# Kernel tuning notes

Hardware: AMD Instinct MI355X
Metric: run time of the kernel (lower is better)

The kernel has to match this reference:

```python
import jax, jax.numpy as jnp
import numpy as np

N_NODES = 50000
BN_EPS = 1e-5


def gcn_conv(x, W, b, src, dst):
    # PyG GCNConv: linear, add self-loops, symmetric degree normalization, scatter-add, bias.
    h = x @ W                                        # [N, D]
    n = x.shape[0]
    deg = jax.ops.segment_sum(jnp.ones(src.shape[0], x.dtype), dst,
                              num_segments=n) + 1.0  # +1 for self-loop
    dinv = jnp.where(deg > 0, jax.lax.rsqrt(deg), 0.0)
    norm = dinv[src] * dinv[dst]                     # [E]
    agg = jax.ops.segment_sum(h[src] * norm[:, None], dst, num_segments=n)
    agg = agg + h * (dinv * dinv)[:, None]           # self-loop contribution
    return agg + b


def batch_norm(x, gamma, beta):
    # training-mode BN over the node axis (biased variance, as torch)
    mu = jnp.mean(x, axis=0)
    var = jnp.mean((x - mu) ** 2, axis=0)
    return (x - mu) * jax.lax.rsqrt(var + BN_EPS) * gamma + beta


def setup_inputs() -> dict:
    key = jax.random.key(0)
    ks = jax.random.split(key, 8)
    D, C = 128, 10
    x = jax.random.normal(ks[0], (N_NODES, D), dtype=jnp.float32)
    edge_index = jax.random.randint(ks[1], (2, 640000), 0, N_NODES, dtype=jnp.int32)
    s = 1.0 / np.sqrt(D)
    return {
        "x": x,
        "edge_index": edge_index,
        "W1": jax.random.normal(ks[2], (D, D), dtype=jnp.float32) * s,
        "b1": jnp.zeros((D,), jnp.float32),
        "gamma1": jnp.ones((D,), jnp.float32),
        "beta1": jnp.zeros((D,), jnp.float32),
        "W2": jax.random.normal(ks[3], (D, D), dtype=jnp.float32) * s,
        "b2": jnp.zeros((D,), jnp.float32),
        "gamma2": jnp.ones((D,), jnp.float32),
        "beta2": jnp.zeros((D,), jnp.float32),
        "lin1_w": jax.random.normal(ks[4], (D, D), dtype=jnp.float32) * s,
        "lin1_b": jnp.zeros((D,), jnp.float32),
        "lin2_w": jax.random.normal(ks[5], (D, C), dtype=jnp.float32) * s,
        "lin2_b": jnp.zeros((C,), jnp.float32),
    }


def reference(x, edge_index, W1, b1, gamma1, beta1, W2, b2, gamma2, beta2,
              lin1_w, lin1_b, lin2_w, lin2_b):
    src, dst = edge_index[0], edge_index[1]
    # layer 1: GCNConv -> ReLU -> BN (dropout = identity at eval)
    h = jax.nn.relu(gcn_conv(x, W1, b1, src, dst))
    h = batch_norm(h, gamma1, beta1)
    # layer 2
    h = jax.nn.relu(gcn_conv(h, W2, b2, src, dst))
    h = batch_norm(h, gamma2, beta2)
    # MLP head
    h = jax.nn.relu(h @ lin1_w + lin1_b)
    logits = h @ lin2_w + lin2_b
    return jax.nn.log_softmax(logits, axis=-1)
```

## Files before the change

### kernel.cpp

```cpp
#include <hip/hip_runtime.h>
#include <hip/hip_bf16.h>
#include <math.h>

typedef unsigned int uint;
typedef unsigned short ushort;
using f32x4 = __attribute__((ext_vector_type(4))) float;
using s16x8 = __attribute__((ext_vector_type(8))) short;

#define NSLOT 64

__device__ __forceinline__ float bflo(uint u) { return __uint_as_float(u << 16); }
__device__ __forceinline__ float bfhi(uint u) { return __uint_as_float(u & 0xffff0000u); }
__device__ __forceinline__ ushort f2bf(float f) {
    uint u = __float_as_uint(f);
    return (ushort)((u + 0x7fffu + ((u >> 16) & 1u)) >> 16);
}
__device__ __forceinline__ float sel4f(float a, float b, float c, float d, int i) {
    float r = a; r = (i == 1) ? b : r; r = (i == 2) ? c : r; r = (i == 3) ? d : r; return r;
}
__device__ __forceinline__ int sel4i(int a, int b, int c, int d, int i) {
    int r = a; r = (i == 1) ? b : r; r = (i == 2) ? c : r; r = (i == 3) ? d : r; return r;
}


__global__ void deg_count(const int* __restrict__ dst, int* __restrict__ deg, int E) {
    int e0 = blockIdx.x * 512 + threadIdx.x;
    int e1 = e0 + 256;
    if (e1 < E) {
        int dA = dst[e0], dB = dst[e1];
        atomicAdd(&deg[dA], 1);
        atomicAdd(&deg[dB], 1);
    } else if (e0 < E) {
        atomicAdd(&deg[dst[e0]], 1);
    }
}

__global__ __launch_bounds__(256) void deg_block_sum(const int* __restrict__ deg,
                                                     int* __restrict__ bsum, int N) {
    __shared__ int s[256];
    int i = blockIdx.x * 256 + threadIdx.x;
    s[threadIdx.x] = (i < N) ? deg[i] : 0;
    __syncthreads();
    #pragma unroll
    for (int off = 128; off > 0; off >>= 1) {
        if (threadIdx.x < off) s[threadIdx.x] += s[threadIdx.x + off];
        __syncthreads();
    }
    if (threadIdx.x == 0) bsum[blockIdx.x] = s[0];
}

__global__ __launch_bounds__(256) void fill_rowstart(const int* __restrict__ deg,
                                                     const int* __restrict__ bsum,
                                                     int* __restrict__ row_start,
                                                     int* __restrict__ cursor,
                                                     float* __restrict__ dinv,
                                                     int N, int E, int nblk) {
    __shared__ int s[256];
    __shared__ int sb[256];
    int t = threadIdx.x;
    int i = blockIdx.x * 256 + t;
    int dg = (i < N) ? deg[i] : 0;
    s[t] = dg;
    sb[t] = (t < nblk) ? bsum[t] : 0;
    __syncthreads();
    for (int off = 1; off < 256; off <<= 1) {
        int v1 = (t >= off) ? s[t - off] : 0;
        int v2 = (t >= off) ? sb[t - off] : 0;
        __syncthreads();
        s[t] += v1;
        sb[t] += v2;
        __syncthreads();
    }
    if (i < N) {
        int boff = (blockIdx.x == 0) ? 0 : sb[blockIdx.x - 1];
        int excl = boff + s[t] - dg;
        row_start[i] = excl;
        cursor[i] = excl;
        dinv[i] = rsqrtf((float)dg + 1.0f);
    }
    if (i == 0) row_start[N] = E;
}

__global__ void csr_fill(const int* __restrict__ src, const int* __restrict__ dst,
                         int* __restrict__ cursor, int* __restrict__ csr_src, int E) {
    int e0 = blockIdx.x * 512 + threadIdx.x;
    int e1 = e0 + 256;
    if (e1 < E) {
        int sA = src[e0], dA = dst[e0];
        int sB = src[e1], dB = dst[e1];
        int pA = atomicAdd(&cursor[dA], 1);
        int pB = atomicAdd(&cursor[dB], 1);
        csr_src[pA] = sA;
        csr_src[pB] = sB;
    } else if (e0 < E) {
        int s = src[e0], d = dst[e0];
        int p = atomicAdd(&cursor[d], 1);
        csr_src[p] = s;
    }
}


__global__ __launch_bounds__(256) void prep_weights(const float* __restrict__ W1,
                                                    const float* __restrict__ W2,
                                                    const float* __restrict__ W3,
                                                    const float* __restrict__ l2w,
                                                    const float* __restrict__ l2b,
                                                    ushort* __restrict__ wt1,
                                                    ushort* __restrict__ wt2,
                                                    ushort* __restrict__ wt3,
                                                    ushort* __restrict__ w2bf,
                                                    float* __restrict__ b2pad) {
    int i = blockIdx.x * 256 + threadIdx.x;
    int li = i & 16383;
    int k = li >> 7, n = li & 127;
    const float* Ws = (i < 16384) ? W1 : (i < 32768) ? W2 : W3;
    ushort* Wd = (i < 16384) ? wt1 : (i < 32768) ? wt2 : wt3;
    Wd[n * 128 + k] = f2bf(Ws[li]);
    if (i < 2048) {
        int c = i >> 7, kk = i & 127;
        float v = (c < 10) ? l2w[kk * 10 + c] : 0.f;
        w2bf[c * 128 + kk] = f2bf(v);
    }
    if (i < 16) b2pad[i] = (i < 10) ? l2b[i] : -1e30f;
}


template<bool XF32, bool AFF, bool PRESCALE, bool HEAD>
__global__ __launch_bounds__(256) void gemm_mfma(const void* __restrict__ Xv,
                                                 const float* __restrict__ scale,
                                                 const float* __restrict__ shift,
                                                 const ushort* __restrict__ Bt,
                                                 const float* __restrict__ bias,
                                                 const float* __restrict__ dinv,
                                                 ushort* __restrict__ Y,
                                                 const ushort* __restrict__ W2bf,
                                                 const float* __restrict__ b2pad,
                                                 float* __restrict__ OUT, int N) {
    __shared__ char smem[2 * 16384 + 32768];
    char* Bl = smem + 32768;

    int tid = threadIdx.x;
    int brow = blockIdx.x * 128;

    {
        int n = tid >> 1, h = tid & 1;
        const uint4* srcp = (const uint4*)(Bt + n * 128 + h * 64);
        #pragma unroll
        for (int i = 0; i < 8; ++i) {
            uint4 v = srcp[i];
            int u = (h * 8 + i) ^ (n & 7);
            *(uint4*)(Bl + n * 256 + u * 16) = v;
        }
    }

    int lane = tid & 63, w = tid >> 6;
    int m = lane & 15, g = lane >> 4;
    int wr = w * 16;

    #pragma unroll
    for (int t = 0; t < 2; ++t) {
        char* Al = smem + t * 16384;
        int rbase = brow + t * 64;

        {
            int r = tid >> 2, c0 = (tid & 3) * 32;
            int row = rbase + r;
            bool ok = row < N;
            uint pk[16];
            if (XF32) {
                const float* Xr = (const float*)Xv + (size_t)row * 128 + c0;
                #pragma unroll
                for (int i = 0; i < 16; ++i) {
                    float f0 = ok ? Xr[i * 2] : 0.f;
                    float f1 = ok ? Xr[i * 2 + 1] : 0.f;
                    pk[i] = (uint)f2bf(f0) | ((uint)f2bf(f1) << 16);
                }
            } else {
                const uint* Xr = (const uint*)((const ushort*)Xv + (size_t)row * 128 + c0);
                #pragma unroll
                for (int i = 0; i < 16; ++i) {
                    uint u = ok ? Xr[i] : 0u;
                    float f0 = bflo(u), f1 = bfhi(u);
                    if (AFF) {
                        int c = c0 + i * 2;
                        f0 = f0 * scale[c] + shift[c];
                        f1 = f1 * scale[c + 1] + shift[c + 1];
                    }
                    pk[i] = (uint)f2bf(f0) | ((uint)f2bf(f1) << 16);
                }
            }
            #pragma unroll
            for (int i = 0; i < 4; ++i) {
                int u = ((tid & 3) * 4 + i) ^ (r & 7);
                *(uint4*)(Al + r * 256 + u * 16) = *(uint4*)&pk[i * 4];
            }
        }
        __syncthreads();

        f32x4 acc[8];
        #pragma unroll
        for (int nt = 0; nt < 8; ++nt) acc[nt] = (f32x4){0.f, 0.f, 0.f, 0.f};

        #pragma unroll
        for (int kk = 0; kk < 4; ++kk) {
            int u = (kk * 4 + g) ^ (m & 7);
            s16x8 a = *(const s16x8*)(Al + (wr + m) * 256 + u * 16);
            #pragma unroll
            for (int nt = 0; nt < 8; ++nt) {
                s16x8 b = *(const s16x8*)(Bl + (nt * 16 + m) * 256 + u * 16);
                acc[nt] = __builtin_amdgcn_mfma_f32_16x16x32_bf16(a, b, acc[nt], 0, 0, 0);
            }
        }

        if (!HEAD) {
            #pragma unroll
            for (int i = 0; i < 4; ++i) {
                int row = rbase + wr + g * 4 + i;
                if (row < N) {
                    float dv = PRESCALE ? dinv[row] : 1.f;
                    #pragma unroll
                    for (int nt = 0; nt < 8; ++nt) {
                        float v = acc[nt][i];
                        if (PRESCALE) v *= dv;
                        Y[(size_t)row * 128 + nt * 16 + m] = f2bf(v);
                    }
                }
            }
        } else {
            float bv[8];
            #pragma unroll
            for (int nt = 0; nt < 8; ++nt) bv[nt] = bias[nt * 16 + m];
            #pragma unroll
            for (int i = 0; i < 4; ++i) {
                int r = wr + g * 4 + i;
                #pragma unroll
                for (int nt = 0; nt < 8; ++nt) {
                    float v = fmaxf(acc[nt][i] + bv[nt], 0.f);
                    int col = nt * 16 + m;
                    int u = (col >> 3) ^ (r & 7);
                    *(ushort*)(Al + r * 256 + u * 16 + (col & 7) * 2) = f2bf(v);
                }
            }
            __syncthreads();
            float b2v = b2pad[m];
            f32x4 lg = (f32x4){b2v, b2v, b2v, b2v};
            #pragma unroll
            for (int kk = 0; kk < 4; ++kk) {
                int u = (kk * 4 + g) ^ (m & 7);
                s16x8 a = *(const s16x8*)(Al + (wr + m) * 256 + u * 16);
                s16x8 b = *(const s16x8*)(&W2bf[m * 128 + (kk * 4 + g) * 8]);
                lg = __builtin_amdgcn_mfma_f32_16x16x32_bf16(a, b, lg, 0, 0, 0);
            }
            #pragma unroll
            for (int i = 0; i < 4; ++i) {
                float v = lg[i];
                float mx = v;
                #pragma unroll
                for (int off = 8; off > 0; off >>= 1) mx = fmaxf(mx, __shfl_xor(mx, off, 64));
                float ex = expf(v - mx);
                float sm = ex;
                #pragma unroll
                for (int off = 8; off > 0; off >>= 1) sm += __shfl_xor(sm, off, 64);
                float res = v - (mx + logf(sm));
                int grow = rbase + wr + g * 4 + i;
                if (m < 10 && grow < N) OUT[(size_t)grow * 10 + m] = res;
            }
        }
    }
}


__global__ __launch_bounds__(256) void gather_fused(const ushort* __restrict__ H,
                                                    const int* __restrict__ row_start,
                                                    const int* __restrict__ csr_src,
                                                    const float* __restrict__ dinv,
                                                    const float* __restrict__ bias,
                                                    ushort* __restrict__ Y,
                                                    float* __restrict__ bnpart, int N) {
    int g = threadIdx.x >> 6, lane = threadIdx.x & 63;
    int d = lane * 2;
    float b0 = bias[d], b1 = bias[d + 1];
    float s0 = 0.f, s1 = 0.f, ss0 = 0.f, ss1 = 0.f;

    int nchunks = (N + 3) / 4;
    int chunk = blockIdx.x * 4 + g;

    if (chunk < nchunks) {
        int c = chunk * 4;
        int nn = min(4, N - c);

        int rsv = row_start[c + min(lane, nn)];
        int rs0 = __shfl(rsv, 0);
        int rs1 = __shfl(rsv, min(1, nn));
        int rs2 = __shfl(rsv, min(2, nn));
        int rs3 = __shfl(rsv, min(3, nn));
        int rs4 = __shfl(rsv, nn);

        float dvv = dinv[c + min(lane, nn - 1)];
        float dv0 = __shfl(dvv, 0);
        float dv1 = __shfl(dvv, min(1, nn - 1));
        float dv2 = __shfl(dvv, min(2, nn - 1));
        float dv3 = __shfl(dvv, min(3, nn - 1));

        uint h0 = *(const uint*)&H[(size_t)c * 128 + d];
        uint h1 = (nn > 1) ? *(const uint*)&H[(size_t)(c + 1) * 128 + d] : 0u;
        uint h2 = (nn > 2) ? *(const uint*)&H[(size_t)(c + 2) * 128 + d] : 0u;
        uint h3 = (nn > 3) ? *(const uint*)&H[(size_t)(c + 3) * 128 + d] : 0u;

        float i0_0 = bflo(h0) * dv0 + b0, i1_0 = bfhi(h0) * dv0 + b1;
        float i0_1 = bflo(h1) * dv1 + b0, i1_1 = bfhi(h1) * dv1 + b1;
        float i0_2 = bflo(h2) * dv2 + b0, i1_2 = bfhi(h2) * dv2 + b1;
        float i0_3 = bflo(h3) * dv3 + b0, i1_3 = bfhi(h3) * dv3 + b1;

        int e0 = rs0, eend = rs4;
        int seg = 0;
        int nextb = rs1;
        float i0s = i0_0, i1s = i1_0, dvs = dv0;
        float es0 = 0.f, es1 = 0.f;

        for (int base = e0; base < eend; base += 64) {
            int cnt = min(64, eend - base);
            int sl = (lane < cnt) ? csr_src[base + lane] : 0;

            for (int j = 0; j < cnt; j += 16) {
                int mm = min(16, cnt - j);
                uint v[16];
                #pragma unroll
                for (int k = 0; k < 16; ++k) {
                    int idx = min(j + k, cnt - 1);
                    int sk = __shfl(sl, idx);
                    v[k] = *(const uint*)&H[(size_t)sk * 128 + d];
                }
                #pragma unroll
                for (int k = 0; k < 16; ++k) {
                    if (k < mm) {
                        int e = base + j + k;
                        while (e >= nextb) {
                            float r0 = fmaxf(es0 * dvs + i0s, 0.f);
                            float r1 = fmaxf(es1 * dvs + i1s, 0.f);
                            *(uint*)&Y[(size_t)(c + seg) * 128 + d] =
                                (uint)f2bf(r0) | ((uint)f2bf(r1) << 16);
                            s0 += r0; ss0 += r0 * r0; s1 += r1; ss1 += r1 * r1;
                            seg++;
                            i0s = sel4f(i0_0, i0_1, i0_2, i0_3, seg);
                            i1s = sel4f(i1_0, i1_1, i1_2, i1_3, seg);
                            dvs = sel4f(dv0, dv1, dv2, dv3, seg);
                            nextb = sel4i(rs1, rs2, rs3, rs4, seg);
                            es0 = 0.f; es1 = 0.f;
                        }
                        es0 += bflo(v[k]);
                        es1 += bfhi(v[k]);
                    }
                }
            }
        }
        for (;;) {
            float r0 = fmaxf(es0 * dvs + i0s, 0.f);
            float r1 = fmaxf(es1 * dvs + i1s, 0.f);
            *(uint*)&Y[(size_t)(c + seg) * 128 + d] = (uint)f2bf(r0) | ((uint)f2bf(r1) << 16);
            s0 += r0; ss0 += r0 * r0; s1 += r1; ss1 += r1 * r1;
            seg++;
            if (seg >= nn) break;
            i0s = sel4f(i0_0, i0_1, i0_2, i0_3, seg);
            i1s = sel4f(i1_0, i1_1, i1_2, i1_3, seg);
            dvs = sel4f(dv0, dv1, dv2, dv3, seg);
            nextb = sel4i(rs1, rs2, rs3, rs4, seg);
            es0 = 0.f; es1 = 0.f;
        }
    }

    float* bp = bnpart + (size_t)(blockIdx.x & (NSLOT - 1)) * 256;
    __shared__ float red[4][128];
    red[g][d] = s0; red[g][d + 1] = s1;
    __syncthreads();
    if (g == 0) {
        atomicAdd(&bp[d],     red[0][d] + red[1][d] + red[2][d] + red[3][d]);
        atomicAdd(&bp[d + 1], red[0][d + 1] + red[1][d + 1] + red[2][d + 1] + red[3][d + 1]);
    }
    __syncthreads();
    red[g][d] = ss0; red[g][d + 1] = ss1;
    __syncthreads();
    if (g == 0) {
        atomicAdd(&bp[128 + d],     red[0][d] + red[1][d] + red[2][d] + red[3][d]);
        atomicAdd(&bp[128 + d + 1], red[0][d + 1] + red[1][d + 1] + red[2][d + 1] + red[3][d + 1]);
    }
}

__global__ void bnfinalize(float* __restrict__ bnpart,
                           const float* __restrict__ gamma, const float* __restrict__ beta,
                           float* __restrict__ scale, float* __restrict__ shift, float invN) {
    int d = threadIdx.x;
    float sum = 0.f, ss = 0.f;
    #pragma unroll 8
    for (int s = 0; s < NSLOT; ++s) {
        sum += bnpart[s * 256 + d];
        ss  += bnpart[s * 256 + 128 + d];
        bnpart[s * 256 + d] = 0.f;
        bnpart[s * 256 + 128 + d] = 0.f;
    }
    float mu  = sum * invN;
    float var = ss * invN - mu * mu;
    float sc  = gamma[d] * rsqrtf(var + 1e-5f);
    scale[d] = sc;
    shift[d] = beta[d] - mu * sc;
}


static inline char* align16(char* p) { return (char*)(((uintptr_t)p + 15) & ~(uintptr_t)15); }

extern "C" void kernel_launch(void* const* d_in, const int* in_sizes, int n_in,
                              void* d_out, int out_size, void* d_ws, size_t ws_size,
                              hipStream_t stream) {
    const float* x    = (const float*)d_in[0];
    const int*   ei   = (const int*)d_in[1];
    const float* W1   = (const float*)d_in[2];
    const float* b1   = (const float*)d_in[3];
    const float* g1   = (const float*)d_in[4];
    const float* be1  = (const float*)d_in[5];
    const float* W2   = (const float*)d_in[6];
    const float* b2   = (const float*)d_in[7];
    const float* g2   = (const float*)d_in[8];
    const float* be2  = (const float*)d_in[9];
    const float* l1w  = (const float*)d_in[10];
    const float* l1b  = (const float*)d_in[11];
    const float* l2w  = (const float*)d_in[12];
    const float* l2b  = (const float*)d_in[13];
    float* out = (float*)d_out;

    int N = in_sizes[0] / 128;
    int E = in_sizes[1] / 2;
    const int* srcp = ei;
    const int* dstp = ei + E;

    char* w = (char*)d_ws;
    ushort* bufA   = (ushort*)w;  w = align16(w + (size_t)N * 128 * 2);
    ushort* bufB   = (ushort*)w;  w = align16(w + (size_t)N * 128 * 2);
    int*   degc    = (int*)w;     w += (size_t)N * 4;
    float* bnpart  = (float*)w;   w = align16(w + (size_t)NSLOT * 256 * 4);
    float* dinv    = (float*)w;   w = align16(w + (size_t)N * 4);
    int*   row_st  = (int*)w;     w = align16(w + (size_t)(N + 1) * 4);
    int*   cursor  = (int*)w;     w = align16(w + (size_t)N * 4);
    int*   bsum    = (int*)w;     w = align16(w + 256 * 4);
    int*   csr_src = (int*)w;     w = align16(w + (size_t)E * 4);
    float* scale   = (float*)w;   w = align16(w + 128 * 4);
    float* shift   = (float*)w;   w = align16(w + 128 * 4);
    ushort* wt1    = (ushort*)w;  w = align16(w + 16384 * 2);
    ushort* wt2    = (ushort*)w;  w = align16(w + 16384 * 2);
    ushort* wt3    = (ushort*)w;  w = align16(w + 16384 * 2);
    ushort* w2bf   = (ushort*)w;  w = align16(w + 2048 * 2);
    float* b2pad   = (float*)w;   w = align16(w + 16 * 4);

    int eg2 = (E + 511) / 512;
    int ng = (N + 255) / 256;
    int gemm_grid = (N + 127) / 128;
    int nchunks = (N + 3) / 4;
    int gather_grid = (nchunks + 3) / 4;

    hipMemsetAsync(degc, 0, ((size_t)N + NSLOT * 256) * 4, stream);
    deg_count<<<eg2, 256, 0, stream>>>(dstp, degc, E);
    deg_block_sum<<<ng, 256, 0, stream>>>(degc, bsum, N);
    fill_rowstart<<<ng, 256, 0, stream>>>(degc, bsum, row_st, cursor, dinv, N, E, ng);
    csr_fill<<<eg2, 256, 0, stream>>>(srcp, dstp, cursor, csr_src, E);
    prep_weights<<<192, 256, 0, stream>>>(W1, W2, l1w, l2w, l2b, wt1, wt2, wt3, w2bf, b2pad);

    gemm_mfma<true, false, true, false><<<gemm_grid, 256, 0, stream>>>(
        x, nullptr, nullptr, wt1, nullptr, dinv, bufA, nullptr, nullptr, nullptr, N);
    gather_fused<<<gather_grid, 256, 0, stream>>>(bufA, row_st, csr_src, dinv, b1, bufB, bnpart, N);
    bnfinalize<<<1, 128, 0, stream>>>(bnpart, g1, be1, scale, shift, 1.0f / N);

    gemm_mfma<false, true, true, false><<<gemm_grid, 256, 0, stream>>>(
        bufB, scale, shift, wt2, nullptr, dinv, bufA, nullptr, nullptr, nullptr, N);
    gather_fused<<<gather_grid, 256, 0, stream>>>(bufA, row_st, csr_src, dinv, b2, bufB, bnpart, N);
    bnfinalize<<<1, 128, 0, stream>>>(bnpart, g2, be2, scale, shift, 1.0f / N);

    gemm_mfma<false, true, false, true><<<gemm_grid, 256, 0, stream>>>(
        bufB, scale, shift, wt3, l1b, nullptr, nullptr, w2bf, b2pad, out, N);
}
```

Before: 323.3 us.

## Cut kernel launches by fusing memset, scan, and BN finalize into neighbouring kernels

Replaces the memset and weight-prep launches with a single init kernel that zeroes the counters and converts the weights. The two scan kernels become one, using a global spin barrier across blocks. BN finalize moves into the gather kernel through a last-block-done counter. Edge kernels now handle four edges per thread. This removes several small launches, but the spin barrier only works if all scan blocks are resident at once, and the last-block reduction adds serial work at the end of the gather.

```diff
diff --git a/kernel.cpp b/kernel.cpp
--- a/kernel.cpp
+++ b/kernel.cpp
@@ -23,94 +23,24 @@
 }
 
 
-__global__ void deg_count(const int* __restrict__ dst, int* __restrict__ deg, int E) {
-    int e0 = blockIdx.x * 512 + threadIdx.x;
-    int e1 = e0 + 256;
-    if (e1 < E) {
-        int dA = dst[e0], dB = dst[e1];
-        atomicAdd(&deg[dA], 1);
-        atomicAdd(&deg[dB], 1);
-    } else if (e0 < E) {
-        atomicAdd(&deg[dst[e0]], 1);
-    }
-}
-
-__global__ __launch_bounds__(256) void deg_block_sum(const int* __restrict__ deg,
-                                                     int* __restrict__ bsum, int N) {
-    __shared__ int s[256];
-    int i = blockIdx.x * 256 + threadIdx.x;
-    s[threadIdx.x] = (i < N) ? deg[i] : 0;
-    __syncthreads();
-    #pragma unroll
-    for (int off = 128; off > 0; off >>= 1) {
-        if (threadIdx.x < off) s[threadIdx.x] += s[threadIdx.x + off];
-        __syncthreads();
-    }
-    if (threadIdx.x == 0) bsum[blockIdx.x] = s[0];
-}
-
-__global__ __launch_bounds__(256) void fill_rowstart(const int* __restrict__ deg,
-                                                     const int* __restrict__ bsum,
-                                                     int* __restrict__ row_start,
-                                                     int* __restrict__ cursor,
-                                                     float* __restrict__ dinv,
-                                                     int N, int E, int nblk) {
-    __shared__ int s[256];
-    __shared__ int sb[256];
-    int t = threadIdx.x;
-    int i = blockIdx.x * 256 + t;
-    int dg = (i < N) ? deg[i] : 0;
-    s[t] = dg;
-    sb[t] = (t < nblk) ? bsum[t] : 0;
-    __syncthreads();
-    for (int off = 1; off < 256; off <<= 1) {
-        int v1 = (t >= off) ? s[t - off] : 0;
-        int v2 = (t >= off) ? sb[t - off] : 0;
-        __syncthreads();
-        s[t] += v1;
-        sb[t] += v2;
-        __syncthreads();
-    }
-    if (i < N) {
-        int boff = (blockIdx.x == 0) ? 0 : sb[blockIdx.x - 1];
-        int excl = boff + s[t] - dg;
-        row_start[i] = excl;
-        cursor[i] = excl;
-        dinv[i] = rsqrtf((float)dg + 1.0f);
-    }
-    if (i == 0) row_start[N] = E;
-}
-
-__global__ void csr_fill(const int* __restrict__ src, const int* __restrict__ dst,
-                         int* __restrict__ cursor, int* __restrict__ csr_src, int E) {
-    int e0 = blockIdx.x * 512 + threadIdx.x;
-    int e1 = e0 + 256;
-    if (e1 < E) {
-        int sA = src[e0], dA = dst[e0];
-        int sB = src[e1], dB = dst[e1];
-        int pA = atomicAdd(&cursor[dA], 1);
-        int pB = atomicAdd(&cursor[dB], 1);
-        csr_src[pA] = sA;
-        csr_src[pB] = sB;
-    } else if (e0 < E) {
-        int s = src[e0], d = dst[e0];
-        int p = atomicAdd(&cursor[d], 1);
-        csr_src[p] = s;
-    }
-}
-
-
-__global__ __launch_bounds__(256) void prep_weights(const float* __restrict__ W1,
-                                                    const float* __restrict__ W2,
-                                                    const float* __restrict__ W3,
-                                                    const float* __restrict__ l2w,
-                                                    const float* __restrict__ l2b,
-                                                    ushort* __restrict__ wt1,
-                                                    ushort* __restrict__ wt2,
-                                                    ushort* __restrict__ wt3,
-                                                    ushort* __restrict__ w2bf,
-                                                    float* __restrict__ b2pad) {
-    int i = blockIdx.x * 256 + threadIdx.x;
+__global__ __launch_bounds__(256) void init_prep(uint4* __restrict__ zbase, int nz, int ZB,
+                                                 const float* __restrict__ W1,
+                                                 const float* __restrict__ W2,
+                                                 const float* __restrict__ W3,
+                                                 const float* __restrict__ l2w,
+                                                 const float* __restrict__ l2b,
+                                                 ushort* __restrict__ wt1,
+                                                 ushort* __restrict__ wt2,
+                                                 ushort* __restrict__ wt3,
+                                                 ushort* __restrict__ w2bf,
+                                                 float* __restrict__ b2pad) {
+    int bid = blockIdx.x;
+    if (bid < ZB) {
+        int i = bid * 256 + threadIdx.x;
+        if (i < nz) zbase[i] = (uint4){0u, 0u, 0u, 0u};
+        return;
+    }
+    int i = (bid - ZB) * 256 + threadIdx.x;
     int li = i & 16383;
     int k = li >> 7, n = li & 127;
     const float* Ws = (i < 16384) ? W1 : (i < 32768) ? W2 : W3;
@@ -122,6 +52,92 @@
         w2bf[c * 128 + kk] = f2bf(v);
     }
     if (i < 16) b2pad[i] = (i < 10) ? l2b[i] : -1e30f;
+}
+
+
+__global__ __launch_bounds__(256) void deg_count(const int* __restrict__ dst,
+                                                 int* __restrict__ deg, int E) {
+    int base = blockIdx.x * 1024 + threadIdx.x;
+    int d[4]; bool ok[4];
+    #pragma unroll
+    for (int k = 0; k < 4; ++k) {
+        int e = base + k * 256;
+        ok[k] = e < E;
+        d[k] = ok[k] ? dst[e] : 0;
+    }
+    #pragma unroll
+    for (int k = 0; k < 4; ++k)
+        if (ok[k]) atomicAdd(&deg[d[k]], 1);
+}
+
+
+__global__ __launch_bounds__(256) void scan_fill(const int* __restrict__ deg,
+                                                 int* __restrict__ bsum,
+                                                 int* __restrict__ sync_ctr,
+                                                 int* __restrict__ row_start,
+                                                 int* __restrict__ cursor,
+                                                 float* __restrict__ dinv,
+                                                 int N, int E, int nblk) {
+    __shared__ int s[256];
+    __shared__ int sb[256];
+    int t = threadIdx.x;
+    int bid = blockIdx.x;
+    int i = bid * 256 + t;
+    int dg = (i < N) ? deg[i] : 0;
+    s[t] = dg;
+    __syncthreads();
+    for (int off = 1; off < 256; off <<= 1) {
+        int v = (t >= off) ? s[t - off] : 0;
+        __syncthreads();
+        s[t] += v;
+        __syncthreads();
+    }
+    if (t == 0) {
+        bsum[bid] = s[255];
+        __threadfence();
+        atomicAdd(sync_ctr, 1);
+        while (atomicAdd(sync_ctr, 0) < nblk) __builtin_amdgcn_s_sleep(8);
+    }
+    __syncthreads();
+    sb[t] = (t < nblk) ? atomicAdd(&bsum[t], 0) : 0;
+    __syncthreads();
+    for (int off = 1; off < 256; off <<= 1) {
+        int v = (t >= off) ? sb[t - off] : 0;
+        __syncthreads();
+        sb[t] += v;
+        __syncthreads();
+    }
+    if (i < N) {
+        int boff = (bid == 0) ? 0 : sb[bid - 1];
+        int excl = boff + s[t] - dg;
+        row_start[i] = excl;
+        cursor[i] = excl;
+        dinv[i] = rsqrtf((float)dg + 1.0f);
+    }
+    if (i == 0) row_start[N] = E;
+}
+
+
+__global__ __launch_bounds__(256) void csr_fill(const int* __restrict__ src,
+                                                const int* __restrict__ dst,
+                                                int* __restrict__ cursor,
+                                                int* __restrict__ csr_src, int E) {
+    int base = blockIdx.x * 1024 + threadIdx.x;
+    int s[4], d[4]; bool ok[4];
+    #pragma unroll
+    for (int k = 0; k < 4; ++k) {
+        int e = base + k * 256;
+        ok[k] = e < E;
+        s[k] = ok[k] ? src[e] : 0;
+        d[k] = ok[k] ? dst[e] : 0;
+    }
+    #pragma unroll
+    for (int k = 0; k < 4; ++k) {
+        if (ok[k]) {
+            int p = atomicAdd(&cursor[d[k]], 1);
+            csr_src[p] = s[k];
+        }
+    }
 }
 
 
@@ -276,7 +292,13 @@
                                                     const float* __restrict__ dinv,
                                                     const float* __restrict__ bias,
                                                     ushort* __restrict__ Y,
-                                                    float* __restrict__ bnpart, int N) {
+                                                    float* __restrict__ bnpart,
+                                                    int* __restrict__ gctr,
+                                                    const float* __restrict__ gamma,
+                                                    const float* __restrict__ beta,
+                                                    float* __restrict__ scale,
+                                                    float* __restrict__ shift,
+                                                    float invN, int N) {
     int g = threadIdx.x >> 6, lane = threadIdx.x & 63;
     int d = lane * 2;
     float b0 = bias[d], b1 = bias[d + 1];
@@ -384,25 +406,33 @@
         atomicAdd(&bp[128 + d],     red[0][d] + red[1][d] + red[2][d] + red[3][d]);
         atomicAdd(&bp[128 + d + 1], red[0][d + 1] + red[1][d + 1] + red[2][d + 1] + red[3][d + 1]);
     }
-}
-
-__global__ void bnfinalize(float* __restrict__ bnpart,
-                           const float* __restrict__ gamma, const float* __restrict__ beta,
-                           float* __restrict__ scale, float* __restrict__ shift, float invN) {
-    int d = threadIdx.x;
-    float sum = 0.f, ss = 0.f;
-    #pragma unroll 8
-    for (int s = 0; s < NSLOT; ++s) {
-        sum += bnpart[s * 256 + d];
-        ss  += bnpart[s * 256 + 128 + d];
-        bnpart[s * 256 + d] = 0.f;
-        bnpart[s * 256 + 128 + d] = 0.f;
-    }
-    float mu  = sum * invN;
-    float var = ss * invN - mu * mu;
-    float sc  = gamma[d] * rsqrtf(var + 1e-5f);
-    scale[d] = sc;
-    shift[d] = beta[d] - mu * sc;
+
+    __threadfence();
+    __shared__ int amLast;
+    if (threadIdx.x == 0) {
+        int old = atomicAdd(gctr, 1);
+        amLast = (old == (int)gridDim.x - 1) ? 1 : 0;
+    }
+    __syncthreads();
+    if (amLast) {
+        int t = threadIdx.x;
+        if (t < 128) {
+            float sum = 0.f, ss = 0.f;
+            #pragma unroll 8
+            for (int s = 0; s < NSLOT; ++s) {
+                sum += atomicAdd(&bnpart[s * 256 + t], 0.f);
+                ss  += atomicAdd(&bnpart[s * 256 + 128 + t], 0.f);
+            }
+            float mu  = sum * invN;
+            float var = ss * invN - mu * mu;
+            float sc  = gamma[t] * rsqrtf(var + 1e-5f);
+            scale[t] = sc;
+            shift[t] = beta[t] - mu * sc;
+        }
+        __syncthreads();
+        for (int i = t; i < NSLOT * 256; i += 256) bnpart[i] = 0.f;
+        if (t == 0) *gctr = 0;
+    }
 }
 
 
@@ -435,8 +465,12 @@
     char* w = (char*)d_ws;
     ushort* bufA   = (ushort*)w;  w = align16(w + (size_t)N * 128 * 2);
     ushort* bufB   = (ushort*)w;  w = align16(w + (size_t)N * 128 * 2);
+    char* zstart   = w;
     int*   degc    = (int*)w;     w += (size_t)N * 4;
-    float* bnpart  = (float*)w;   w = align16(w + (size_t)NSLOT * 256 * 4);
+    float* bnpart  = (float*)w;   w += (size_t)NSLOT * 256 * 4;
+    int*   ctrs    = (int*)w;     w += 16;
+    size_t zbytes  = (size_t)(w - zstart);
+    w = align16(w);
     float* dinv    = (float*)w;   w = align16(w + (size_t)N * 4);
     int*   row_st  = (int*)w;     w = align16(w + (size_t)(N + 1) * 4);
     int*   cursor  = (int*)w;     w = align16(w + (size_t)N * 4);
@@ -450,28 +484,30 @@
     ushort* w2bf   = (ushort*)w;  w = align16(w + 2048 * 2);
     float* b2pad   = (float*)w;   w = align16(w + 16 * 4);
 
-    int eg2 = (E + 511) / 512;
+    int nz = (int)(zbytes / 16);
+    int ZB = (nz + 255) / 256;
+    int eg4 = (E + 1023) / 1024;
     int ng = (N + 255) / 256;
     int gemm_grid = (N + 127) / 128;
     int nchunks = (N + 3) / 4;
     int gather_grid = (nchunks + 3) / 4;
-
-    hipMemsetAsync(degc, 0, ((size_t)N + NSLOT * 256) * 4, stream);
-    deg_count<<<eg2, 256, 0, stream>>>(dstp, degc, E);
-    deg_block_sum<<<ng, 256, 0, stream>>>(degc, bsum, N);
-    fill_rowstart<<<ng, 256, 0, stream>>>(degc, bsum, row_st, cursor, dinv, N, E, ng);
-    csr_fill<<<eg2, 256, 0, stream>>>(srcp, dstp, cursor, csr_src, E);
-    prep_weights<<<192, 256, 0, stream>>>(W1, W2, l1w, l2w, l2b, wt1, wt2, wt3, w2bf, b2pad);
+    float invN = 1.0f / (float)N;
+
+    init_prep<<<ZB + 192, 256, 0, stream>>>((uint4*)zstart, nz, ZB,
+                                            W1, W2, l1w, l2w, l2b, wt1, wt2, wt3, w2bf, b2pad);
+    deg_count<<<eg4, 256, 0, stream>>>(dstp, degc, E);
+    scan_fill<<<ng, 256, 0, stream>>>(degc, bsum, &ctrs[0], row_st, cursor, dinv, N, E, ng);
+    csr_fill<<<eg4, 256, 0, stream>>>(srcp, dstp, cursor, csr_src, E);
 
     gemm_mfma<true, false, true, false><<<gemm_grid, 256, 0, stream>>>(
         x, nullptr, nullptr, wt1, nullptr, dinv, bufA, nullptr, nullptr, nullptr, N);
-    gather_fused<<<gather_grid, 256, 0, stream>>>(bufA, row_st, csr_src, dinv, b1, bufB, bnpart, N);
-    bnfinalize<<<1, 128, 0, stream>>>(bnpart, g1, be1, scale, shift, 1.0f / N);
+    gather_fused<<<gather_grid, 256, 0, stream>>>(bufA, row_st, csr_src, dinv, b1, bufB,
+                                                  bnpart, &ctrs[1], g1, be1, scale, shift, invN, N);
 
     gemm_mfma<false, true, true, false><<<gemm_grid, 256, 0, stream>>>(
         bufB, scale, shift, wt2, nullptr, dinv, bufA, nullptr, nullptr, nullptr, N);
-    gather_fused<<<gather_grid, 256, 0, stream>>>(bufA, row_st, csr_src, dinv, b2, bufB, bnpart, N);
-    bnfinalize<<<1, 128, 0, stream>>>(bnpart, g2, be2, scale, shift, 1.0f / N);
+    gather_fused<<<gather_grid, 256, 0, stream>>>(bufA, row_st, csr_src, dinv, b2, bufB,
+                                                  bnpart, &ctrs[1], g2, be2, scale, shift, invN, N);
 
     gemm_mfma<false, true, false, true><<<gemm_grid, 256, 0, stream>>>(
         bufB, scale, shift, wt3, l1b, nullptr, nullptr, w2bf, b2pad, out, N);
```

After: 868.1 us. 2.69x slower.
